# Kernel tuning notes

Hardware: AMD Instinct MI355X
Metric: run time of the kernel (lower is better)

The kernel has to match this reference:

```python
import jax, jax.numpy as jnp
import numpy as np

B, N_ELEM, N_NODES, E2 = 4096, 2048, 1024, 4096


def setup_inputs() -> dict:
    key = jax.random.key(0)
    k = jax.random.split(key, 7)
    return {
        "EA": jax.random.normal(k[0], (B, N_ELEM), dtype=jnp.float32),
        "e": jax.random.normal(k[1], (B, N_ELEM), dtype=jnp.float32),
        "q": jax.random.normal(k[2], (B, N_NODES, 2), dtype=jnp.float32),
        "r": jax.random.normal(k[3], (B, N_NODES, 2), dtype=jnp.float32),
        "vecs": jax.random.normal(k[4], (E2, 2), dtype=jnp.float32),
        "node_ids": jax.random.randint(k[5], (E2,), 0, N_NODES, dtype=jnp.int32),
        "elem_ids": jax.random.randint(k[6], (E2,), 0, N_ELEM, dtype=jnp.int32),
    }


def reference(EA, e, q, r, vecs, node_ids, elem_ids):
    # axial_forces = EA * e : [B, N_ELEM]
    axial = EA * e
    # gather per incidence entry and scale by the 2-vector: [B, E2, 2]
    contrib = axial[:, elem_ids][..., None] * vecs[None, :, :]
    n_sample, n_nodes = q.shape[0], q.shape[1]
    # scatter-add contributions into per-node residual: [B, N_NODES, 2]
    residual = jnp.zeros((n_sample, n_nodes, 2), dtype=EA.dtype)
    residual = residual.at[:, node_ids, :].add(contrib)
    residual = residual - q - r
    return jnp.mean(jnp.square(residual))
```

## Files before the change

kernel.cpp:

```cpp
#include <hip/hip_runtime.h>

#define B_SAMPLES 4096
#define N_ELEM    2048
#define N_NODES   1024
#define E2        4096
#define BLOCK     256
#define MBLOCK    512
#define SLOTS     32
#define S         8
#define MAIN_BLOCKS (B_SAMPLES / S)

#define WS_CNT_OFF    0
#define WS_ELLW_OFF   4096
#define WS_ELLID_OFF  (4096 + SLOTS * N_NODES * 8)
#define WS_PART_OFF   (WS_ELLID_OFF + SLOTS * N_NODES * 4)

__host__ __device__ __forceinline__ int swz_eid(int eid) {
    return ((eid & 3) << 9) | (eid >> 2);
}

__global__ __launch_bounds__(BLOCK) void neq_zero_kernel(
    float2* __restrict__ ellw, int* __restrict__ ellid, int* __restrict__ cnt)
{
    const int i = blockIdx.x * BLOCK + threadIdx.x;
    ellw[i] = make_float2(0.f, 0.f);
    ellid[i] = 0;
    if (i < N_NODES) cnt[i] = 0;
}

__global__ __launch_bounds__(BLOCK) void neq_build_kernel(
    const float* __restrict__ vecs, const int* __restrict__ node_ids,
    const int* __restrict__ elem_ids, int* __restrict__ cnt,
    float2* __restrict__ ellw, int* __restrict__ ellid)
{
    const int j = blockIdx.x * BLOCK + threadIdx.x;
    int nid = node_ids[j];
    int sid = swz_eid(elem_ids[j]);
    float2 v = ((const float2*)vecs)[j];
    int slot = atomicAdd(&cnt[nid], 1);
    if (slot < SLOTS) {
        ellw[slot * N_NODES + nid] = v;
        ellid[slot * N_NODES + nid] = sid;
    }
}

#define FMA4(A, V, W) do { (A).x += (V).x * (W); (A).y += (V).y * (W); \
                           (A).z += (V).z * (W); (A).w += (V).w * (W); } while (0)

__global__ __launch_bounds__(MBLOCK, 4) void neq_main_kernel(
    const float* __restrict__ EA, const float* __restrict__ e,
    const float* __restrict__ q,  const float* __restrict__ r,
    const int* __restrict__ cnt, const float2* __restrict__ ellw,
    const int* __restrict__ ellid, float* __restrict__ partial)
{
    __shared__ float4 axialA[N_ELEM];
    __shared__ float4 axialB[N_ELEM];
    __shared__ float red[MBLOCK / 64];

    const int b0 = blockIdx.x * S;
    const int t = threadIdx.x;

    const float4* EA4 = (const float4*)(EA + (size_t)b0 * N_ELEM);
    const float4* e4  = (const float4*)(e  + (size_t)b0 * N_ELEM);
    float4 ea0 = EA4[0 * 512 + t];
    float4 ea1 = EA4[1 * 512 + t];
    float4 ea2 = EA4[2 * 512 + t];
    float4 ea3 = EA4[3 * 512 + t];
    float4 me0 = e4 [0 * 512 + t];
    float4 me1 = e4 [1 * 512 + t];
    float4 me2 = e4 [2 * 512 + t];
    float4 me3 = e4 [3 * 512 + t];

    int c0n = min(cnt[t], SLOTS);
    int c1n = min(cnt[t + 512], SLOTS);
    int kmax = max(c0n, c1n);

    {
        float4 p0, p1, p2, p3;
        p0.x = ea0.x * me0.x; p0.y = ea0.y * me0.y; p0.z = ea0.z * me0.z; p0.w = ea0.w * me0.w;
        p1.x = ea1.x * me1.x; p1.y = ea1.y * me1.y; p1.z = ea1.z * me1.z; p1.w = ea1.w * me1.w;
        p2.x = ea2.x * me2.x; p2.y = ea2.y * me2.y; p2.z = ea2.z * me2.z; p2.w = ea2.w * me2.w;
        p3.x = ea3.x * me3.x; p3.y = ea3.y * me3.y; p3.z = ea3.z * me3.z; p3.w = ea3.w * me3.w;
        axialA[t]        = make_float4(p0.x, p1.x, p2.x, p3.x);
        axialA[512 + t]  = make_float4(p0.y, p1.y, p2.y, p3.y);
        axialA[1024 + t] = make_float4(p0.z, p1.z, p2.z, p3.z);
        axialA[1536 + t] = make_float4(p0.w, p1.w, p2.w, p3.w);
    }
    {
        float4 fa0 = EA4[4 * 512 + t];
        float4 fa1 = EA4[5 * 512 + t];
        float4 fa2 = EA4[6 * 512 + t];
        float4 fa3 = EA4[7 * 512 + t];
        float4 fm0 = e4 [4 * 512 + t];
        float4 fm1 = e4 [5 * 512 + t];
        float4 fm2 = e4 [6 * 512 + t];
        float4 fm3 = e4 [7 * 512 + t];
        float4 p0, p1, p2, p3;
        p0.x = fa0.x * fm0.x; p0.y = fa0.y * fm0.y; p0.z = fa0.z * fm0.z; p0.w = fa0.w * fm0.w;
        p1.x = fa1.x * fm1.x; p1.y = fa1.y * fm1.y; p1.z = fa1.z * fm1.z; p1.w = fa1.w * fm1.w;
        p2.x = fa2.x * fm2.x; p2.y = fa2.y * fm2.y; p2.z = fa2.z * fm2.z; p2.w = fa2.w * fm2.w;
        p3.x = fa3.x * fm3.x; p3.y = fa3.y * fm3.y; p3.z = fa3.z * fm3.z; p3.w = fa3.w * fm3.w;
        axialB[t]        = make_float4(p0.x, p1.x, p2.x, p3.x);
        axialB[512 + t]  = make_float4(p0.y, p1.y, p2.y, p3.y);
        axialB[1024 + t] = make_float4(p0.z, p1.z, p2.z, p3.z);
        axialB[1536 + t] = make_float4(p0.w, p1.w, p2.w, p3.w);
    }
    __syncthreads();

    float4 xA0 = make_float4(0.f, 0.f, 0.f, 0.f);
    float4 yA0 = make_float4(0.f, 0.f, 0.f, 0.f);
    float4 xB0 = make_float4(0.f, 0.f, 0.f, 0.f);
    float4 yB0 = make_float4(0.f, 0.f, 0.f, 0.f);
    float4 xA1 = make_float4(0.f, 0.f, 0.f, 0.f);
    float4 yA1 = make_float4(0.f, 0.f, 0.f, 0.f);
    float4 xB1 = make_float4(0.f, 0.f, 0.f, 0.f);
    float4 yB1 = make_float4(0.f, 0.f, 0.f, 0.f);

    for (int k = 0; k < kmax; ++k) {
        const float2* rw  = ellw  + (size_t)k * N_NODES;
        const int*    rid = ellid + (size_t)k * N_NODES;
        float2 w0 = rw[t];
        float2 w1 = rw[t + 512];
        int i0 = rid[t];
        int i1 = rid[t + 512];
        float4 A0 = axialA[i0];
        float4 B0 = axialB[i0];
        float4 A1 = axialA[i1];
        float4 B1 = axialB[i1];
        FMA4(xA0, A0, w0.x);  FMA4(yA0, A0, w0.y);
        FMA4(xB0, B0, w0.x);  FMA4(yB0, B0, w0.y);
        FMA4(xA1, A1, w1.x);  FMA4(yA1, A1, w1.y);
        FMA4(xB1, B1, w1.x);  FMA4(yB1, B1, w1.y);
    }

    float acc = 0.f;
#pragma unroll
    for (int s = 0; s < 4; ++s) {
        const float2* q2 = (const float2*)(q + (size_t)(b0 + s) * N_NODES * 2);
        const float2* r2 = (const float2*)(r + (size_t)(b0 + s) * N_NODES * 2);
        float2 qa = q2[t],       ra = r2[t];
        float2 qb = q2[t + 512], rb = r2[t + 512];
        float ax0 = (s == 0) ? xA0.x : (s == 1) ? xA0.y : (s == 2) ? xA0.z : xA0.w;
        float ay0 = (s == 0) ? yA0.x : (s == 1) ? yA0.y : (s == 2) ? yA0.z : yA0.w;
        float ax1 = (s == 0) ? xA1.x : (s == 1) ? xA1.y : (s == 2) ? xA1.z : xA1.w;
        float ay1 = (s == 0) ? yA1.x : (s == 1) ? yA1.y : (s == 2) ? yA1.z : yA1.w;
        float x = ax0 - qa.x - ra.x;
        float y = ay0 - qa.y - ra.y;
        acc += x * x + y * y;
        x = ax1 - qb.x - rb.x;
        y = ay1 - qb.y - rb.y;
        acc += x * x + y * y;
    }
#pragma unroll
    for (int s = 0; s < 4; ++s) {
        const float2* q2 = (const float2*)(q + (size_t)(b0 + 4 + s) * N_NODES * 2);
        const float2* r2 = (const float2*)(r + (size_t)(b0 + 4 + s) * N_NODES * 2);
        float2 qa = q2[t],       ra = r2[t];
        float2 qb = q2[t + 512], rb = r2[t + 512];
        float ax0 = (s == 0) ? xB0.x : (s == 1) ? xB0.y : (s == 2) ? xB0.z : xB0.w;
        float ay0 = (s == 0) ? yB0.x : (s == 1) ? yB0.y : (s == 2) ? yB0.z : yB0.w;
        float ax1 = (s == 0) ? xB1.x : (s == 1) ? xB1.y : (s == 2) ? xB1.z : xB1.w;
        float ay1 = (s == 0) ? yB1.x : (s == 1) ? yB1.y : (s == 2) ? yB1.z : yB1.w;
        float x = ax0 - qa.x - ra.x;
        float y = ay0 - qa.y - ra.y;
        acc += x * x + y * y;
        x = ax1 - qb.x - rb.x;
        y = ay1 - qb.y - rb.y;
        acc += x * x + y * y;
    }

#pragma unroll
    for (int off = 32; off > 0; off >>= 1)
        acc += __shfl_down(acc, off, 64);
    if ((t & 63) == 0) red[t >> 6] = acc;
    __syncthreads();
    if (t == 0) {
        float s = 0.f;
#pragma unroll
        for (int w = 0; w < MBLOCK / 64; ++w) s += red[w];
        partial[blockIdx.x] = s;
    }
}

__global__ __launch_bounds__(512) void neq_reduce_kernel(
    const float* __restrict__ partial, float* __restrict__ out)
{
    __shared__ float red[512 / 64];
    const int t = threadIdx.x;
    float acc = partial[t];
#pragma unroll
    for (int off = 32; off > 0; off >>= 1)
        acc += __shfl_down(acc, off, 64);
    if ((t & 63) == 0) red[t >> 6] = acc;
    __syncthreads();
    if (t == 0) {
        float s = 0.f;
#pragma unroll
        for (int w = 0; w < 512 / 64; ++w) s += red[w];
        const float inv_n = 1.0f / (float)((size_t)B_SAMPLES * N_NODES * 2);
        out[0] = s * inv_n;
    }
}

extern "C" void kernel_launch(void* const* d_in, const int* in_sizes, int n_in,
                              void* d_out, int out_size, void* d_ws, size_t ws_size,
                              hipStream_t stream) {
    const float* EA       = (const float*)d_in[0];
    const float* e        = (const float*)d_in[1];
    const float* q        = (const float*)d_in[2];
    const float* r        = (const float*)d_in[3];
    const float* vecs     = (const float*)d_in[4];
    const int*   node_ids = (const int*)d_in[5];
    const int*   elem_ids = (const int*)d_in[6];

    char* ws = (char*)d_ws;
    int*    cnt     = (int*)(ws + WS_CNT_OFF);
    float2* ellw    = (float2*)(ws + WS_ELLW_OFF);
    int*    ellid   = (int*)(ws + WS_ELLID_OFF);
    float*  partial = (float*)(ws + WS_PART_OFF);

    neq_zero_kernel<<<(SLOTS * N_NODES) / BLOCK, BLOCK, 0, stream>>>(ellw, ellid, cnt);
    neq_build_kernel<<<E2 / BLOCK, BLOCK, 0, stream>>>(
        vecs, node_ids, elem_ids, cnt, ellw, ellid);
    neq_main_kernel<<<MAIN_BLOCKS, MBLOCK, 0, stream>>>(
        EA, e, q, r, cnt, ellw, ellid, partial);
    neq_reduce_kernel<<<1, 512, 0, stream>>>(partial, (float*)d_out);
}
```

Baseline: 163.3 us.

## Replace ELL incidence table with CSR built in one block, staged in LDS

The padded ELL incidence layout (32 slots per node, zeroed each call) is replaced by a compact CSR built in a single 1024-thread block using a shared-memory histogram, prefix scan and scatter. The zero kernel goes away, and the main kernel copies the full CSR weights and ids into LDS so the inner loop reads them from shared memory instead of global memory. This raises LDS use per block, so occupancy is lowered to 2 blocks per SM. It also drops the 32-slot cap, and the single-block build runs serially on one CU.

```diff
diff --git a/kernel.cpp b/kernel.cpp
--- a/kernel.cpp
+++ b/kernel.cpp
@@ -4,78 +4,117 @@
 #define N_ELEM    2048
 #define N_NODES   1024
 #define E2        4096
-#define BLOCK     256
 #define MBLOCK    512
-#define SLOTS     32
 #define S         8
 #define MAIN_BLOCKS (B_SAMPLES / S)
 
-#define WS_CNT_OFF    0
-#define WS_ELLW_OFF   4096
-#define WS_ELLID_OFF  (4096 + SLOTS * N_NODES * 8)
-#define WS_PART_OFF   (WS_ELLID_OFF + SLOTS * N_NODES * 4)
+#define WS_OFFS_OFF   0
+#define WS_CSRW_OFF   8192
+#define WS_CSRID_OFF  (8192 + E2 * 8)
+#define WS_PART_OFF   (WS_CSRID_OFF + E2 * 4)
 
 __host__ __device__ __forceinline__ int swz_eid(int eid) {
     return ((eid & 3) << 9) | (eid >> 2);
 }
 
-__global__ __launch_bounds__(BLOCK) void neq_zero_kernel(
-    float2* __restrict__ ellw, int* __restrict__ ellid, int* __restrict__ cnt)
+__global__ __launch_bounds__(1024) void neq_build_kernel(
+    const float* __restrict__ vecs, const int* __restrict__ node_ids,
+    const int* __restrict__ elem_ids,
+    int* __restrict__ offs, float2* __restrict__ csrw, int* __restrict__ csrid)
 {
-    const int i = blockIdx.x * BLOCK + threadIdx.x;
-    ellw[i] = make_float2(0.f, 0.f);
-    ellid[i] = 0;
-    if (i < N_NODES) cnt[i] = 0;
-}
-
-__global__ __launch_bounds__(BLOCK) void neq_build_kernel(
-    const float* __restrict__ vecs, const int* __restrict__ node_ids,
-    const int* __restrict__ elem_ids, int* __restrict__ cnt,
-    float2* __restrict__ ellw, int* __restrict__ ellid)
-{
-    const int j = blockIdx.x * BLOCK + threadIdx.x;
-    int nid = node_ids[j];
-    int sid = swz_eid(elem_ids[j]);
-    float2 v = ((const float2*)vecs)[j];
-    int slot = atomicAdd(&cnt[nid], 1);
-    if (slot < SLOTS) {
-        ellw[slot * N_NODES + nid] = v;
-        ellid[slot * N_NODES + nid] = sid;
+    __shared__ int scnt[N_NODES];
+    __shared__ int soff[N_NODES];
+    __shared__ int wsum[16];
+    const int t = threadIdx.x;
+    const int lane = t & 63, wid = t >> 6;
+
+    scnt[t] = 0;
+    __syncthreads();
+#pragma unroll
+    for (int i = 0; i < 4; ++i)
+        atomicAdd(&scnt[node_ids[t + i * 1024]], 1);
+    __syncthreads();
+
+    int c = scnt[t];
+    int v = c;
+#pragma unroll
+    for (int off = 1; off < 64; off <<= 1) {
+        int u = __shfl_up(v, off, 64);
+        if (lane >= off) v += u;
+    }
+    if (lane == 63) wsum[wid] = v;
+    __syncthreads();
+    if (wid == 0) {
+        int s = (lane < 16) ? wsum[lane] : 0;
+#pragma unroll
+        for (int off = 1; off < 16; off <<= 1) {
+            int u = __shfl_up(s, off, 64);
+            if (lane >= off) s += u;
+        }
+        if (lane < 16) wsum[lane] = s;
+    }
+    __syncthreads();
+    int wbase = (wid == 0) ? 0 : wsum[wid - 1];
+    int excl = wbase + v - c;
+    soff[t] = excl;
+    offs[t] = excl;
+    if (t == 1023) offs[1024] = excl + c;
+    __syncthreads();
+
+    scnt[t] = 0;
+    __syncthreads();
+#pragma unroll
+    for (int i = 0; i < 4; ++i) {
+        int j = t + i * 1024;
+        int nid = node_ids[j];
+        int slot = atomicAdd(&scnt[nid], 1);
+        int pos = soff[nid] + slot;
+        csrw[pos] = ((const float2*)vecs)[j];
+        csrid[pos] = swz_eid(elem_ids[j]);
     }
 }
 
 #define FMA4(A, V, W) do { (A).x += (V).x * (W); (A).y += (V).y * (W); \
                            (A).z += (V).z * (W); (A).w += (V).w * (W); } while (0)
 
-__global__ __launch_bounds__(MBLOCK, 4) void neq_main_kernel(
+__global__ __launch_bounds__(MBLOCK, 2) void neq_main_kernel(
     const float* __restrict__ EA, const float* __restrict__ e,
     const float* __restrict__ q,  const float* __restrict__ r,
-    const int* __restrict__ cnt, const float2* __restrict__ ellw,
-    const int* __restrict__ ellid, float* __restrict__ partial)
+    const int* __restrict__ offs, const float2* __restrict__ csrw,
+    const int* __restrict__ csrid, float* __restrict__ partial)
 {
     __shared__ float4 axialA[N_ELEM];
     __shared__ float4 axialB[N_ELEM];
-    __shared__ float red[MBLOCK / 64];
+    __shared__ float2 wlds[E2];
+    __shared__ int    ilds[E2];
+    __shared__ float  red[MBLOCK / 64];
 
     const int b0 = blockIdx.x * S;
     const int t = threadIdx.x;
 
+#pragma unroll
+    for (int i = 0; i < 8; ++i) {
+        wlds[t + i * 512] = csrw[t + i * 512];
+        ilds[t + i * 512] = csrid[t + i * 512];
+    }
+
+    int o0 = offs[t];
+    int c0 = offs[t + 1] - o0;
+    int o1 = offs[t + 512];
+    int c1 = offs[t + 513] - o1;
+    int kmax = max(c0, c1);
+
     const float4* EA4 = (const float4*)(EA + (size_t)b0 * N_ELEM);
     const float4* e4  = (const float4*)(e  + (size_t)b0 * N_ELEM);
-    float4 ea0 = EA4[0 * 512 + t];
-    float4 ea1 = EA4[1 * 512 + t];
-    float4 ea2 = EA4[2 * 512 + t];
-    float4 ea3 = EA4[3 * 512 + t];
-    float4 me0 = e4 [0 * 512 + t];
-    float4 me1 = e4 [1 * 512 + t];
-    float4 me2 = e4 [2 * 512 + t];
-    float4 me3 = e4 [3 * 512 + t];
-
-    int c0n = min(cnt[t], SLOTS);
-    int c1n = min(cnt[t + 512], SLOTS);
-    int kmax = max(c0n, c1n);
-
     {
+        float4 ea0 = EA4[0 * 512 + t];
+        float4 ea1 = EA4[1 * 512 + t];
+        float4 ea2 = EA4[2 * 512 + t];
+        float4 ea3 = EA4[3 * 512 + t];
+        float4 me0 = e4 [0 * 512 + t];
+        float4 me1 = e4 [1 * 512 + t];
+        float4 me2 = e4 [2 * 512 + t];
+        float4 me3 = e4 [3 * 512 + t];
         float4 p0, p1, p2, p3;
         p0.x = ea0.x * me0.x; p0.y = ea0.y * me0.y; p0.z = ea0.z * me0.z; p0.w = ea0.w * me0.w;
         p1.x = ea1.x * me1.x; p1.y = ea1.y * me1.y; p1.z = ea1.z * me1.z; p1.w = ea1.w * me1.w;
@@ -117,16 +156,18 @@
     float4 yB1 = make_float4(0.f, 0.f, 0.f, 0.f);
 
     for (int k = 0; k < kmax; ++k) {
-        const float2* rw  = ellw  + (size_t)k * N_NODES;
-        const int*    rid = ellid + (size_t)k * N_NODES;
-        float2 w0 = rw[t];
-        float2 w1 = rw[t + 512];
-        int i0 = rid[t];
-        int i1 = rid[t + 512];
-        float4 A0 = axialA[i0];
-        float4 B0 = axialB[i0];
-        float4 A1 = axialA[i1];
-        float4 B1 = axialB[i1];
+        int i0 = min(o0 + k, E2 - 1);
+        int i1 = min(o1 + k, E2 - 1);
+        float2 w0 = wlds[i0];
+        float2 w1 = wlds[i1];
+        int id0 = ilds[i0];
+        int id1 = ilds[i1];
+        if (k >= c0) w0 = make_float2(0.f, 0.f);
+        if (k >= c1) w1 = make_float2(0.f, 0.f);
+        float4 A0 = axialA[id0];
+        float4 B0 = axialB[id0];
+        float4 A1 = axialA[id1];
+        float4 B1 = axialB[id1];
         FMA4(xA0, A0, w0.x);  FMA4(yA0, A0, w0.y);
         FMA4(xB0, B0, w0.x);  FMA4(yB0, B0, w0.y);
         FMA4(xA1, A1, w1.x);  FMA4(yA1, A1, w1.y);
@@ -214,15 +255,14 @@
     const int*   elem_ids = (const int*)d_in[6];
 
     char* ws = (char*)d_ws;
-    int*    cnt     = (int*)(ws + WS_CNT_OFF);
-    float2* ellw    = (float2*)(ws + WS_ELLW_OFF);
-    int*    ellid   = (int*)(ws + WS_ELLID_OFF);
+    int*    offs    = (int*)(ws + WS_OFFS_OFF);
+    float2* csrw    = (float2*)(ws + WS_CSRW_OFF);
+    int*    csrid   = (int*)(ws + WS_CSRID_OFF);
     float*  partial = (float*)(ws + WS_PART_OFF);
 
-    neq_zero_kernel<<<(SLOTS * N_NODES) / BLOCK, BLOCK, 0, stream>>>(ellw, ellid, cnt);
-    neq_build_kernel<<<E2 / BLOCK, BLOCK, 0, stream>>>(
-        vecs, node_ids, elem_ids, cnt, ellw, ellid);
+    neq_build_kernel<<<1, 1024, 0, stream>>>(
+        vecs, node_ids, elem_ids, offs, csrw, csrid);
     neq_main_kernel<<<MAIN_BLOCKS, MBLOCK, 0, stream>>>(
-        EA, e, q, r, cnt, ellw, ellid, partial);
+        EA, e, q, r, offs, csrw, csrid, partial);
     neq_reduce_kernel<<<1, 512, 0, stream>>>(partial, (float*)d_out);
 }
```

New measurement: 171.0 us. 4.8% more time.
